# Kernel optimization log

Hardware: AMD Instinct MI355X
Metric: run time of the kernel (lower is better)

## Reference

```python
import jax, jax.numpy as jnp
import numpy as np

HID = 2048
NH = 16
HD = HID // NH  # 128
EPS = 1e-6
BASE = 10000.0


def _rmsnorm(x, w):
    xf = x.astype(jnp.float32)
    y = xf * jax.lax.rsqrt(jnp.mean(xf * xf, axis=-1, keepdims=True) + EPS)
    return y.astype(x.dtype) * w


def _rope_cos_sin(seq_len, dtype):
    inv_freq = 1.0 / (BASE ** (jnp.arange(0, HD, 2, dtype=jnp.float32) / HD))
    t = jnp.arange(seq_len, dtype=jnp.float32)
    freqs = jnp.outer(t, inv_freq)          # [S, HD/2]
    emb = jnp.concatenate([freqs, freqs], axis=-1)  # [S, HD]
    return jnp.cos(emb).astype(dtype), jnp.sin(emb).astype(dtype)


def _rotate_half(x):
    x1, x2 = jnp.split(x, 2, axis=-1)
    return jnp.concatenate([-x2, x1], axis=-1)


def setup_inputs() -> dict:
    key = jax.random.key(0)
    ks = jax.random.split(key, 8)
    B, S = 2, 2048
    s = 0.02
    return {
        "hidden_states": jax.random.normal(ks[0], (B, S, HID), jnp.float32),
        "Wq": jax.random.normal(ks[1], (HID, HID), jnp.float32) * s,
        "Wk": jax.random.normal(ks[2], (HID, HID), jnp.float32) * s,
        "Wv": jax.random.normal(ks[3], (HID, HID), jnp.float32) * s,
        "Wo": jax.random.normal(ks[4], (HID, HID), jnp.float32) * s,
        "w1": jax.random.normal(ks[5], (HID, HID), jnp.float32) * s,
        "w2": jax.random.normal(ks[6], (HID, HID), jnp.float32) * s,
        "w3": jax.random.normal(ks[7], (HID, HID), jnp.float32) * s,
        "ln1_w": jnp.ones((HID,), jnp.float32),
        "ln2_w": jnp.ones((HID,), jnp.float32),
    }


def reference(hidden_states, Wq, Wk, Wv, Wo, w1, w2, w3, ln1_w, ln2_w):
    B, S, _ = hidden_states.shape
    residual = hidden_states
    x = _rmsnorm(hidden_states, ln1_w)

    # projections -> [B, NH, S, HD]
    q = (x @ Wq).reshape(B, S, NH, HD).transpose(0, 2, 1, 3)
    k = (x @ Wk).reshape(B, S, NH, HD).transpose(0, 2, 1, 3)
    v = (x @ Wv).reshape(B, S, NH, HD).transpose(0, 2, 1, 3)

    cos, sin = _rope_cos_sin(S, x.dtype)  # [S, HD]
    cos = cos[None, None]  # broadcast over batch and heads
    sin = sin[None, None]
    q = q * cos + _rotate_half(q) * sin
    k = k * cos + _rotate_half(k) * sin

    scores = jnp.einsum("bhqd,bhkd->bhqk", q, k) / np.sqrt(HD).astype(np.float32)
    # no attention_mask (torch default path). fp32 softmax.
    attn = jax.nn.softmax(scores.astype(jnp.float32), axis=-1).astype(q.dtype)
    ctx = jnp.einsum("bhqk,bhkd->bhqd", attn, v)  # [B, NH, S, HD]
    ctx = ctx.transpose(0, 2, 1, 3).reshape(B, S, HID)
    attn_out = ctx @ Wo

    h = residual + attn_out
    residual = h
    y = _rmsnorm(h, ln2_w)
    mlp = (jax.nn.silu(y @ w1) * (y @ w3)) @ w2
    return residual + mlp
```

## Files before the change

### kernel.cpp

```cpp
#include <hip/hip_runtime.h>

#define HIDN 2048
#define NHEAD 16
#define HD 128
#define SEQ 2048
#define BATCH 2
#define NROWS (BATCH*SEQ)

typedef __bf16 bf16_t;
typedef bf16_t bf16x8 __attribute__((ext_vector_type(8)));
typedef float f32x4 __attribute__((ext_vector_type(4)));

#define AS1 __attribute__((address_space(1)))
#define AS3 __attribute__((address_space(3)))

__device__ __forceinline__ unsigned short f2bf(float x) {
  union { bf16_t b; unsigned short u; } cv; cv.b = (bf16_t)x; return cv.u;
}

#define MFMA16(a,b,c) __builtin_amdgcn_mfma_f32_16x16x32_bf16((a),(b),(c),0,0,0)

__device__ __forceinline__ void gload16(const void* g, void* l) {
  __builtin_amdgcn_global_load_lds((const AS1 void*)g, (AS3 void*)l, 16, 0, 0);
}

__global__ __launch_bounds__(256) void transpose_all_kernel(
    const float* __restrict__ Wq, const float* __restrict__ Wk,
    const float* __restrict__ Wv, const float* __restrict__ Wo,
    const float* __restrict__ w1, const float* __restrict__ w3,
    const float* __restrict__ w2, unsigned short* __restrict__ wblk) {
  const int z = blockIdx.z;
  const float* W; unsigned short* dstb; int tmode = 0, half = 0;
  switch (z) {
    case 0: W = Wq; dstb = wblk;                       tmode = 1; break;
    case 1: W = Wk; dstb = wblk + (size_t)2048 * HIDN; tmode = 1; break;
    case 2: W = Wv; dstb = wblk + (size_t)4096 * HIDN; break;
    case 3: W = Wo; dstb = wblk + (size_t)6144 * HIDN; break;
    case 4: W = w1; dstb = wblk + (size_t)8192 * HIDN; tmode = 2; half = 0; break;
    case 5: W = w3; dstb = wblk + (size_t)8192 * HIDN; tmode = 2; half = 1; break;
    default: W = w2; dstb = wblk + (size_t)12288 * HIDN; break;
  }
  __shared__ float t[64][69];
  const int tid = threadIdx.x;
  const int bn = blockIdx.x * 64, bk = blockIdx.y * 64;
  const int lc = (tid & 15) * 4, lrw = tid >> 4;
#pragma unroll
  for (int i = 0; i < 4; ++i) {
    int k = bk + lrw + i * 16;
    float4 v = *(const float4*)(W + (long)k * HIDN + bn + lc);
    t[lrw + i * 16][lc] = v.x; t[lrw + i * 16][lc + 1] = v.y;
    t[lrw + i * 16][lc + 2] = v.z; t[lrw + i * 16][lc + 3] = v.w;
  }
  __syncthreads();
  const int nl = tid >> 2, k0 = (tid & 3) * 16;
  int n = bn + nl;
  int dst;
  if (tmode == 0) dst = n;
  else if (tmode == 1) { int d = n & 127; dst = (n & ~127) | ((d & 63) << 1) | (d >> 6); }
  else dst = (n >> 4) * 32 + half * 16 + (n & 15);
  unsigned short* orow = dstb + (long)dst * HIDN + bk + k0;
#pragma unroll
  for (int j = 0; j < 16; j += 4) {
    ushort4 o;
    o.x = f2bf(t[k0 + j][nl]);     o.y = f2bf(t[k0 + j + 1][nl]);
    o.z = f2bf(t[k0 + j + 2][nl]); o.w = f2bf(t[k0 + j + 3][nl]);
    *(ushort4*)(orow + j) = o;
  }
}

__global__ void rope_table_kernel(float* __restrict__ cosT, float* __restrict__ sinT) {
  int s = blockIdx.x, d = threadIdx.x;
  float invf = powf(10000.0f, (-2.0f * (float)d) / 128.0f);
  float ang = (float)s * invf;
  cosT[s * 64 + d] = cosf(ang);
  sinT[s * 64 + d] = sinf(ang);
}

__global__ __launch_bounds__(256) void rmsnorm_kernel(
    const float* __restrict__ x, const float* __restrict__ w, unsigned short* __restrict__ out) {
  long row = blockIdx.x;
  const float* xr = x + row * HIDN;
  int c0 = threadIdx.x * 4;
  float4 v0 = *(const float4*)(xr + c0);
  float4 v1 = *(const float4*)(xr + 1024 + c0);
  float s = v0.x*v0.x + v0.y*v0.y + v0.z*v0.z + v0.w*v0.w
          + v1.x*v1.x + v1.y*v1.y + v1.z*v1.z + v1.w*v1.w;
#pragma unroll
  for (int off = 1; off < 64; off <<= 1) s += __shfl_xor(s, off);
  __shared__ float red[4];
  if ((threadIdx.x & 63) == 0) red[threadIdx.x >> 6] = s;
  __syncthreads();
  float tot = red[0] + red[1] + red[2] + red[3];
  float r = 1.0f / sqrtf(tot * (1.0f / (float)HIDN) + 1e-6f);
  float4 w0 = *(const float4*)(w + c0);
  float4 w1 = *(const float4*)(w + 1024 + c0);
  ushort4 o0, o1;
  o0.x = f2bf(v0.x * r * w0.x); o0.y = f2bf(v0.y * r * w0.y);
  o0.z = f2bf(v0.z * r * w0.z); o0.w = f2bf(v0.w * r * w0.w);
  o1.x = f2bf(v1.x * r * w1.x); o1.y = f2bf(v1.y * r * w1.y);
  o1.z = f2bf(v1.z * r * w1.z); o1.w = f2bf(v1.w * r * w1.w);
  *(ushort4*)(out + row * HIDN + c0) = o0;
  *(ushort4*)(out + row * HIDN + 1024 + c0) = o1;
}

template <int MODE>
__global__ __launch_bounds__(512, 2) void gemm256_kernel(
    const unsigned short* __restrict__ A, const unsigned short* __restrict__ Bt,
    int nbx,
    void* __restrict__ p0, void* __restrict__ p1, void* __restrict__ p2,
    const float* __restrict__ cosT, const float* __restrict__ sinT) {
  __shared__ unsigned short L[65536];
  const int tid = threadIdx.x;
  const int wave = tid >> 6, lane = tid & 63;
  const int lr = lane & 15, lkg = lane >> 4;
  const int wr = wave >> 2, wc = wave & 3;
  const int x7 = lr & 7;
  const int nwg = (int)gridDim.x;
  const int bid = (int)blockIdx.x;
  const int wg = (bid & 7) * (nwg >> 3) + (bid >> 3);
  const int bx = wg % nbx, by = wg / nbx;
  const long bm = (long)by * 256, bn = (long)bx * 256;
  const int sslot = (lane & 7) ^ (lane >> 3);
  const unsigned short* Ag = A + (bm + wave * 8 + (lane >> 3)) * HIDN + sslot * 8;
  const unsigned short* Bg = Bt + (bn + wave * 8 + (lane >> 3)) * HIDN + sslot * 8;
  const char* Lc = (const char*)L;
  f32x4 acc[8][4] = {};
  bf16x8 af[2][2], bfr[4][2];

#define STG(b, mat, half, tile)                                                   \
  {                                                                               \
    const unsigned short* gsrc = ((mat) ? Bg : Ag) + ((long)(half) * 128) * HIDN + (long)(tile) * 64; \
    unsigned short* ldst = &L[((4 * (b) + 2 * (mat) + (half)) * 8192) + wave * 8 * 64]; \
    gload16(gsrc, ldst);                                                          \
    gload16(gsrc + (long)64 * HIDN, ldst + 4096);                                 \
  }
#define DSRA(b, q)                                                                \
  { _Pragma("unroll") for (int mm = 0; mm < 2; ++mm) {                            \
      int row128 = ((q) * 2 + mm) * 16 + lr;                                      \
      _Pragma("unroll") for (int ks = 0; ks < 2; ++ks) {                          \
        int s = ks * 4 + lkg;                                                     \
        af[mm][ks] = *(const bf16x8*)(Lc + (4 * (b) + wr) * 16384 + row128 * 128 + ((s ^ x7) << 4)); \
      } } }
#define DSRB(b)                                                                   \
  { _Pragma("unroll") for (int n = 0; n < 4; ++n) {                               \
      int row128 = (wc & 1) * 64 + n * 16 + lr;                                   \
      _Pragma("unroll") for (int ks = 0; ks < 2; ++ks) {                          \
        int s = ks * 4 + lkg;                                                     \
        bfr[n][ks] = *(const bf16x8*)(Lc + (4 * (b) + 2 + (wc >> 1)) * 16384 + row128 * 128 + ((s ^ x7) << 4)); \
      } } }
#define MFMAQ(q)                                                                  \
  { __builtin_amdgcn_s_setprio(1);                                                \
    _Pragma("unroll") for (int mm = 0; mm < 2; ++mm)                              \
      _Pragma("unroll") for (int n = 0; n < 4; ++n) {                             \
        acc[(q) * 2 + mm][n] = MFMA16(af[mm][0], bfr[n][0], acc[(q) * 2 + mm][n]); \
        acc[(q) * 2 + mm][n] = MFMA16(af[mm][1], bfr[n][1], acc[(q) * 2 + mm][n]); \
      }                                                                           \
    __builtin_amdgcn_s_setprio(0); }
#define BARR __builtin_amdgcn_s_barrier()
#define LGK0 { asm volatile("s_waitcnt lgkmcnt(0)" ::: "memory"); __builtin_amdgcn_sched_barrier(0); }

  STG(0, 0, 0, 0); STG(0, 0, 1, 0); STG(0, 1, 0, 0); STG(0, 1, 1, 0);
  STG(1, 1, 0, 1); STG(1, 1, 1, 1); STG(1, 0, 0, 1);
  asm volatile("s_waitcnt vmcnt(6)" ::: "memory");
  __builtin_amdgcn_sched_barrier(0);
  BARR;

  const int NIT = HIDN / 128;
#pragma unroll 1
  for (int i = 0; i < NIT; ++i) {
    const int t2 = 2 * i + 2, t3 = 2 * i + 3;
    const bool nl_ = (i < NIT - 1);
    DSRA(0, 0); DSRB(0);
    STG(1, 0, 1, 2 * i + 1);
    asm volatile("s_waitcnt lgkmcnt(8)" ::: "memory");
    BARR; LGK0; MFMAQ(0); BARR;
    DSRA(0, 1);
    if (nl_) STG(0, 1, 0, t2);
    BARR; LGK0; MFMAQ(1); BARR;
    DSRA(0, 2);
    if (nl_) STG(0, 1, 1, t2);
    BARR; LGK0; MFMAQ(2); BARR;
    DSRA(0, 3);
    BARR; LGK0; MFMAQ(3);
    if (nl_) { asm volatile("s_waitcnt vmcnt(4)" ::: "memory"); }
    else     { asm volatile("s_waitcnt vmcnt(0)" ::: "memory"); }
    __builtin_amdgcn_sched_barrier(0);
    BARR;
    DSRA(1, 0); DSRB(1);
    if (nl_) STG(0, 0, 0, t2);
    asm volatile("s_waitcnt lgkmcnt(8)" ::: "memory");
    BARR; LGK0; MFMAQ(0); BARR;
    DSRA(1, 1);
    if (nl_) { STG(0, 0, 1, t2); STG(1, 1, 0, t3); }
    BARR; LGK0; MFMAQ(1); BARR;
    DSRA(1, 2);
    if (nl_) STG(1, 1, 1, t3);
    BARR; LGK0; MFMAQ(2); BARR;
    DSRA(1, 3);
    if (nl_) STG(1, 0, 0, t3);
    BARR; LGK0; MFMAQ(3);
    if (nl_) { asm volatile("s_waitcnt vmcnt(6)" ::: "memory"); __builtin_amdgcn_sched_barrier(0); }
    BARR;
  }
#undef STG
#undef DSRA
#undef DSRB
#undef MFMAQ
#undef BARR
#undef LGK0

  const int gc0 = (int)bn + wc * 64;
  if (MODE == 1) {
    unsigned short* bout = (unsigned short*)p0;
#pragma unroll
    for (int m = 0; m < 8; ++m) {
      long r0 = bm + wr * 128 + m * 16 + lkg * 4;
#pragma unroll
      for (int n = 0; n < 4; n += 2) {
        int ggrp = (gc0 + n * 16) >> 5;
        long c = (long)ggrp * 16 + lr;
#pragma unroll
        for (int r = 0; r < 4; ++r) {
          float x = acc[m][n][r], g = acc[m][n + 1][r];
          float sv = x / (1.0f + __expf(-x)) * g;
          bout[(r0 + r) * 2048 + c] = f2bf(sv);
        }
      }
    }
  } else {
    int bufid = gc0 >> 11;
    if (bufid == 2) {
      unsigned short* vT = (unsigned short*)p2;
#pragma unroll
      for (int m = 0; m < 8; ++m) {
        long r0 = bm + wr * 128 + m * 16 + lkg * 4;
        long bq = r0 >> 11;
        int s = (int)(r0 & 2047);
#pragma unroll
        for (int n = 0; n < 4; ++n) {
          int wcol = (gc0 + n * 16 + lr) & 2047;
          int hh = wcol >> 7, dd = wcol & 127;
          ushort4 pw;
          pw.x = f2bf(acc[m][n][0]); pw.y = f2bf(acc[m][n][1]);
          pw.z = f2bf(acc[m][n][2]); pw.w = f2bf(acc[m][n][3]);
          *(ushort4*)(vT + ((bq * 16 + hh) * 128 + dd) * (long)SEQ + s) = pw;
        }
      }
    } else {
      unsigned short* dst = (bufid == 0) ? (unsigned short*)p0 : (unsigned short*)p1;
      const float qscale = (bufid == 0) ? 0.08838834764831845f : 1.0f;
#pragma unroll
      for (int m = 0; m < 8; ++m) {
        long r0 = bm + wr * 128 + m * 16 + lkg * 4;
#pragma unroll
        for (int n = 0; n < 4; ++n) {
          int wcol = (gc0 + n * 16 + lr) & 2047;
          int f = wcol & 127, hh = wcol >> 7;
          int j = f >> 1, odd = f & 1;
          int oc = hh * 128 + (odd ? 64 : 0) + j;
#pragma unroll
          for (int r = 0; r < 4; ++r) {
            long row = r0 + r;
            int s = (int)(row & (SEQ - 1));
            float cv = cosT[s * 64 + j], sn = sinT[s * 64 + j];
            float v = acc[m][n][r];
            float o = __shfl_xor(v, 1);
            float res = (odd ? (v * cv + o * sn) : (v * cv - o * sn)) * qscale;
            dst[row * 2048 + oc] = f2bf(res);
          }
        }
      }
    }
  }
}

template <int MODE>
__global__ __launch_bounds__(256) void gemm_kernel(
    const unsigned short* __restrict__ A, const unsigned short* __restrict__ Bt, int N,
    void* __restrict__ p0, const void* __restrict__ p1) {
  __shared__ unsigned short As[128 * 32];
  __shared__ unsigned short Bs[128 * 32];
  const int tid = threadIdx.x;
  const int lane = tid & 63, wave = tid >> 6;
  const int wm = (wave >> 1) * 64, wn = (wave & 1) * 64;
  const int lr = lane & 15, lkg = lane >> 4;
  const long bm = (long)blockIdx.y * 128, bn = (long)blockIdx.x * 128;
  f32x4 acc[4][4] = {};
  const int rA0 = wave * 32 + (lane >> 2);
  const int gs0 = (lane & 3) ^ ((rA0 >> 1) & 3);
  const int gs1 = (lane & 3) ^ (((rA0 + 16) >> 1) & 3);
  const unsigned short* Ag0 = A + (bm + rA0) * HIDN + gs0 * 8;
  const unsigned short* Ag1 = A + (bm + rA0 + 16) * HIDN + gs1 * 8;
  const unsigned short* Bg0 = Bt + (bn + rA0) * HIDN + gs0 * 8;
  const unsigned short* Bg1 = Bt + (bn + rA0 + 16) * HIDN + gs1 * 8;
  unsigned short* lA0 = &As[(wave * 32) * 32];
  unsigned short* lA1 = &As[(wave * 32 + 16) * 32];
  unsigned short* lB0 = &Bs[(wave * 32) * 32];
  unsigned short* lB1 = &Bs[(wave * 32 + 16) * 32];
  for (int k0 = 0; k0 < HIDN; k0 += 32) {
    __syncthreads();
    gload16(Ag0 + k0, lA0);
    gload16(Ag1 + k0, lA1);
    gload16(Bg0 + k0, lB0);
    gload16(Bg1 + k0, lB1);
    __syncthreads();
    bf16x8 af[4], bfr[4];
#pragma unroll
    for (int m = 0; m < 4; ++m) {
      int row = wm + m * 16 + lr;
      af[m] = *(const bf16x8*)((const char*)As + row * 64 + ((lkg ^ ((row >> 1) & 3)) << 4));
    }
#pragma unroll
    for (int n = 0; n < 4; ++n) {
      int row = wn + n * 16 + lr;
      bfr[n] = *(const bf16x8*)((const char*)Bs + row * 64 + ((lkg ^ ((row >> 1) & 3)) << 4));
    }
#pragma unroll
    for (int m = 0; m < 4; ++m)
#pragma unroll
      for (int n = 0; n < 4; ++n) acc[m][n] = MFMA16(af[m], bfr[n], acc[m][n]);
  }
  float* fout = (float*)p0;
  const float* addsrc = (const float*)p1;
#pragma unroll
  for (int m = 0; m < 4; ++m)
#pragma unroll
    for (int n = 0; n < 4; ++n) {
      long r0 = bm + wm + m * 16 + lkg * 4;
      long c = bn + wn + n * 16 + lr;
#pragma unroll
      for (int r = 0; r < 4; ++r) {
        long idx = (r0 + r) * 2048 + c;
        if (MODE == 2) fout[idx] = addsrc[idx] + acc[m][n][r];
        else fout[idx] = fout[idx] + acc[m][n][r];
      }
    }
}

__global__ __launch_bounds__(256) void flash_attn_kernel(
    const unsigned short* __restrict__ Q, const unsigned short* __restrict__ Kb,
    const unsigned short* __restrict__ vT, unsigned short* __restrict__ O) {
  __shared__ unsigned short Ks[2][64 * 128];
  __shared__ unsigned short Vs[2][128 * 64];
  __shared__ unsigned short Ps[4][16][72];
  const int qt = blockIdx.x, h = blockIdx.y, b = blockIdx.z;
  const int tid = threadIdx.x, wave = tid >> 6, lane = tid & 63;
  const int lr = lane & 15, lkg = lane >> 4, lk = lkg * 8;
  const long rowbase = (long)b * SEQ;
  const int qrow0 = qt * 64 + wave * 16;
  bf16x8 aq[4];
#pragma unroll
  for (int ks = 0; ks < 4; ++ks)
    aq[ks] = *(const bf16x8*)(Q + (rowbase + qrow0 + lr) * HIDN + h * HD + ks * 32 + lk);
  const unsigned short* vbase = vT + ((long)(b * 16 + h) * 128) * SEQ;
  const int krl = lane >> 4;
  const int vrl = lane >> 3, vch = lane & 7;
  f32x4 acc[8] = {};
  float m_ = -3.0e38f, l_ = 0.f;

#define STAGEKV(t_, kv0_)                                                          \
  {                                                                                \
    _Pragma("unroll")                                                              \
    for (int j = 0; j < 4; ++j) {                                                  \
      int rl = wave * 16 + j * 4 + krl;                                            \
      int slot = (lane & 15) ^ (rl & 15);                                          \
      gload16(Kb + (rowbase + (kv0_) + rl) * HIDN + h * HD + slot * 8,             \
              &Ks[(t_) & 1][(wave * 16 + j * 4) * 128]);                           \
    }                                                                              \
    _Pragma("unroll")                                                              \
    for (int j = 0; j < 4; ++j) {                                                  \
      int dd = wave * 32 + j * 8 + vrl;                                            \
      int slot = vch ^ (dd & 7);                                                   \
      gload16(vbase + (long)dd * SEQ + (kv0_) + slot * 8,                          \
              &Vs[(t_) & 1][(wave * 32 + j * 8) * 64]);                            \
    }                                                                              \
  }

  STAGEKV(0, 0);

  for (int t = 0; t < SEQ / 64; ++t) {
    asm volatile("s_waitcnt vmcnt(0)" ::: "memory");
    asm volatile("s_barrier" ::: "memory");
    if (t + 1 < SEQ / 64) STAGEKV(t + 1, (long)(t + 1) * 64);
    const char* ksb = (const char*)Ks[t & 1];
    f32x4 sa[4] = {};
#pragma unroll
    for (int n = 0; n < 4; ++n) {
      int row = n * 16 + lr;
#pragma unroll
      for (int ks = 0; ks < 4; ++ks) {
        bf16x8 bk = *(const bf16x8*)(ksb + row * 256 + (((ks * 4 + lkg) ^ (row & 15)) << 4));
        sa[n] = MFMA16(bk, aq[ks], sa[n]);
      }
    }
    float pmax = sa[0][0];
#pragma unroll
    for (int n = 0; n < 4; ++n)
#pragma unroll
      for (int r = 0; r < 4; ++r) pmax = fmaxf(pmax, sa[n][r]);
    pmax = fmaxf(pmax, __shfl_xor(pmax, 16));
    pmax = fmaxf(pmax, __shfl_xor(pmax, 32));
    if (__all(pmax - m_ <= 8.0f)) {
      float psum = 0.f;
#pragma unroll
      for (int n = 0; n < 4; ++n)
#pragma unroll
        for (int r = 0; r < 4; ++r) {
          float p = __expf(sa[n][r] - m_);
          sa[n][r] = p;
          psum += p;
        }
      psum += __shfl_xor(psum, 16);
      psum += __shfl_xor(psum, 32);
      l_ += psum;
    } else {
      float mnew = fmaxf(m_, pmax);
      float corr = __expf(m_ - mnew);
      float psum = 0.f;
#pragma unroll
      for (int n = 0; n < 4; ++n)
#pragma unroll
        for (int r = 0; r < 4; ++r) {
          float p = __expf(sa[n][r] - mnew);
          sa[n][r] = p;
          psum += p;
        }
      psum += __shfl_xor(psum, 16);
      psum += __shfl_xor(psum, 32);
      l_ = l_ * corr + psum;
      m_ = mnew;
      float corr4[4];
#pragma unroll
      for (int r = 0; r < 4; ++r) corr4[r] = __shfl(corr, 4 * lkg + r);
#pragma unroll
      for (int df = 0; df < 8; ++df)
#pragma unroll
        for (int r = 0; r < 4; ++r) acc[df][r] *= corr4[r];
    }
#pragma unroll
    for (int n = 0; n < 4; ++n) {
      ushort4 pw;
      pw.x = f2bf(sa[n][0]); pw.y = f2bf(sa[n][1]);
      pw.z = f2bf(sa[n][2]); pw.w = f2bf(sa[n][3]);
      *(ushort4*)&Ps[wave][lr][n * 16 + 4 * lkg] = pw;
    }
    bf16x8 pa0 = *(const bf16x8*)&Ps[wave][lr][lk];
    bf16x8 pa1 = *(const bf16x8*)&Ps[wave][lr][32 + lk];
    const char* vsb = (const char*)Vs[t & 1];
#pragma unroll
    for (int df = 0; df < 8; ++df) {
      int row = df * 16 + lr;
      int x7 = row & 7;
      bf16x8 bv0 = *(const bf16x8*)(vsb + row * 128 + ((lkg ^ x7) << 4));
      bf16x8 bv1 = *(const bf16x8*)(vsb + row * 128 + (((4 + lkg) ^ x7) << 4));
      acc[df] = MFMA16(pa0, bv0, acc[df]);
      acc[df] = MFMA16(pa1, bv1, acc[df]);
    }
    asm volatile("s_barrier" ::: "memory");
  }
#undef STAGEKV
  float invl = 1.0f / l_;
  float invl4[4];
#pragma unroll
  for (int r = 0; r < 4; ++r) invl4[r] = __shfl(invl, 4 * lkg + r);
#pragma unroll
  for (int r = 0; r < 4; ++r) {
    long orow = rowbase + qrow0 + lkg * 4 + r;
#pragma unroll
    for (int df = 0; df < 8; ++df)
      O[orow * HIDN + h * HD + df * 16 + lr] = f2bf(acc[df][r] * invl4[r]);
  }
}

extern "C" void kernel_launch(void* const* d_in, const int* in_sizes, int n_in,
                              void* d_out, int out_size, void* d_ws, size_t ws_size,
                              hipStream_t stream) {
  const float* hidden = (const float*)d_in[0];
  const float* Wq = (const float*)d_in[1];
  const float* Wk = (const float*)d_in[2];
  const float* Wv = (const float*)d_in[3];
  const float* Wo = (const float*)d_in[4];
  const float* w1 = (const float*)d_in[5];
  const float* w2 = (const float*)d_in[6];
  const float* w3 = (const float*)d_in[7];
  const float* ln1 = (const float*)d_in[8];
  const float* ln2 = (const float*)d_in[9];
  float* out = (float*)d_out;

  char* ws = (char*)d_ws;
  size_t off = 0;
  auto alloc = [&](size_t bytes) -> void* {
    void* p = ws + off;
    off += (bytes + 255) & ~(size_t)255;
    return p;
  };
  unsigned short* wblk = (unsigned short*)alloc((size_t)(2048L * 6 + 2048) * HIDN * 2);
  unsigned short* wQ = wblk;
  unsigned short* wG = wblk + (size_t)8192 * HIDN;
  unsigned short* wO = wblk + (size_t)6144 * HIDN;
  unsigned short* wD = wblk + (size_t)12288 * HIDN;
  unsigned short* xb   = (unsigned short*)alloc((size_t)NROWS * HIDN * 2);
  unsigned short* qb   = (unsigned short*)alloc((size_t)NROWS * HIDN * 2);
  unsigned short* kb   = (unsigned short*)alloc((size_t)NROWS * HIDN * 2);
  unsigned short* vTb  = (unsigned short*)alloc((size_t)NROWS * HIDN * 2);
  unsigned short* ctxb = (unsigned short*)alloc((size_t)NROWS * HIDN * 2);
  float* cosT = (float*)alloc((size_t)SEQ * 64 * 4);
  float* sinT = (float*)alloc((size_t)SEQ * 64 * 4);
  if (off > ws_size) return;

  transpose_all_kernel<<<dim3(HIDN / 64, HIDN / 64, 7), 256, 0, stream>>>(
      Wq, Wk, Wv, Wo, w1, w3, w2, wblk);
  rope_table_kernel<<<SEQ, 64, 0, stream>>>(cosT, sinT);

  rmsnorm_kernel<<<NROWS, 256, 0, stream>>>(hidden, ln1, xb);

  gemm256_kernel<0><<<(6144 / 256) * (NROWS / 256), 512, 0, stream>>>(
      xb, wQ, 6144 / 256, qb, kb, vTb, cosT, sinT);

  flash_attn_kernel<<<dim3(SEQ / 64, NHEAD, BATCH), 256, 0, stream>>>(qb, kb, vTb, ctxb);

  gemm_kernel<2><<<dim3(2048 / 128, NROWS / 128), 256, 0, stream>>>(
      ctxb, wO, 2048, out, hidden);

  rmsnorm_kernel<<<NROWS, 256, 0, stream>>>(out, ln2, xb);

  gemm256_kernel<1><<<(4096 / 256) * (NROWS / 256), 512, 0, stream>>>(
      xb, wG, 4096 / 256, qb, nullptr, nullptr, nullptr, nullptr);

  gemm_kernel<3><<<dim3(2048 / 128, NROWS / 128), 256, 0, stream>>>(
      qb, wD, 2048, out, nullptr);
}
```

Baseline: 463.7 us.

## Restructure flash attention staging through registers, use exp2 softmax, remap blocks

Moves K/V staging off the direct global-to-LDS loads and onto register prefetch into a single LDS buffer. Shared memory is halved, and launch_bounds(256,3) asks for more resident blocks per CU. The Q scale now folds in log2(e), so softmax can use exp2f instead of __expf, and the rescale threshold is adjusted to match. Blocks are launched as a 1D grid with a remap that spreads consecutive block IDs across an 8-way interleave, likely for XCD/L2 locality. The trade-off is extra register pressure and an additional barrier per tile.

Result: no change. 463.6 us (-0.0%).

```diff
diff --git a/kernel.cpp b/kernel.cpp
--- a/kernel.cpp
+++ b/kernel.cpp
@@ -248,7 +248,7 @@
       }
     } else {
       unsigned short* dst = (bufid == 0) ? (unsigned short*)p0 : (unsigned short*)p1;
-      const float qscale = (bufid == 0) ? 0.08838834764831845f : 1.0f;
+      const float qscale = (bufid == 0) ? 0.12751689f : 1.0f;
 #pragma unroll
       for (int m = 0; m < 8; ++m) {
         long r0 = bm + wr * 128 + m * 16 + lkg * 4;
@@ -337,13 +337,15 @@
     }
 }
 
-__global__ __launch_bounds__(256) void flash_attn_kernel(
+__global__ __launch_bounds__(256, 3) void flash_attn_kernel(
     const unsigned short* __restrict__ Q, const unsigned short* __restrict__ Kb,
     const unsigned short* __restrict__ vT, unsigned short* __restrict__ O) {
-  __shared__ unsigned short Ks[2][64 * 128];
-  __shared__ unsigned short Vs[2][128 * 64];
+  __shared__ unsigned short Ks[64 * 128];
+  __shared__ unsigned short Vs[128 * 64];
   __shared__ unsigned short Ps[4][16][72];
-  const int qt = blockIdx.x, h = blockIdx.y, b = blockIdx.z;
+  const int bid = (int)blockIdx.x;
+  const int wg = (bid & 7) * 128 + (bid >> 3);
+  const int qt = wg & 31, h = (wg >> 5) & 15, b = wg >> 9;
   const int tid = threadIdx.x, wave = tid >> 6, lane = tid & 63;
   const int lr = lane & 15, lkg = lane >> 4, lk = lkg * 8;
   const long rowbase = (long)b * SEQ;
@@ -353,36 +355,41 @@
   for (int ks = 0; ks < 4; ++ks)
     aq[ks] = *(const bf16x8*)(Q + (rowbase + qrow0 + lr) * HIDN + h * HD + ks * 32 + lk);
   const unsigned short* vbase = vT + ((long)(b * 16 + h) * 128) * SEQ;
-  const int krl = lane >> 4;
-  const int vrl = lane >> 3, vch = lane & 7;
+  const int kr_ = tid >> 4, kc_ = tid & 15;
+  const int vd_ = tid >> 3, vc_ = tid & 7;
+  int4 kreg[4], vreg[4];
   f32x4 acc[8] = {};
   float m_ = -3.0e38f, l_ = 0.f;
 
-#define STAGEKV(t_, kv0_)                                                          \
-  {                                                                                \
+#define GLOADKV(kv0_)                                                              \
+  { _Pragma("unroll")                                                              \
+    for (int j = 0; j < 4; ++j)                                                    \
+      kreg[j] = *(const int4*)(Kb + (rowbase + (kv0_) + kr_ + j * 16) * HIDN + h * HD + kc_ * 8); \
     _Pragma("unroll")                                                              \
+    for (int j = 0; j < 4; ++j)                                                    \
+      vreg[j] = *(const int4*)(vbase + (long)(vd_ + j * 32) * SEQ + (kv0_) + vc_ * 8); }
+#define DSWRITEKV()                                                                \
+  { _Pragma("unroll")                                                              \
     for (int j = 0; j < 4; ++j) {                                                  \
-      int rl = wave * 16 + j * 4 + krl;                                            \
-      int slot = (lane & 15) ^ (rl & 15);                                          \
-      gload16(Kb + (rowbase + (kv0_) + rl) * HIDN + h * HD + slot * 8,             \
-              &Ks[(t_) & 1][(wave * 16 + j * 4) * 128]);                           \
+      int row = kr_ + j * 16;                                                      \
+      *(int4*)((char*)Ks + row * 256 + ((kc_ ^ (row & 15)) << 4)) = kreg[j];       \
     }                                                                              \
     _Pragma("unroll")                                                              \
     for (int j = 0; j < 4; ++j) {                                                  \
-      int dd = wave * 32 + j * 8 + vrl;                                            \
-      int slot = vch ^ (dd & 7);                                                   \
-      gload16(vbase + (long)dd * SEQ + (kv0_) + slot * 8,                          \
-              &Vs[(t_) & 1][(wave * 32 + j * 8) * 64]);                            \
-    }                                                                              \
-  }
-
-  STAGEKV(0, 0);
+      int d = vd_ + j * 32;                                                        \
+      *(int4*)((char*)Vs + d * 128 + ((vc_ ^ (d & 7)) << 4)) = vreg[j];            \
+    } }
+
+  GLOADKV(0);
+  asm volatile("s_waitcnt vmcnt(0)" ::: "memory");
+  DSWRITEKV();
+  asm volatile("s_waitcnt lgkmcnt(0)" ::: "memory");
+  __builtin_amdgcn_sched_barrier(0);
+  asm volatile("s_barrier" ::: "memory");
 
   for (int t = 0; t < SEQ / 64; ++t) {
-    asm volatile("s_waitcnt vmcnt(0)" ::: "memory");
-    asm volatile("s_barrier" ::: "memory");
-    if (t + 1 < SEQ / 64) STAGEKV(t + 1, (long)(t + 1) * 64);
-    const char* ksb = (const char*)Ks[t & 1];
+    if (t + 1 < SEQ / 64) GLOADKV((long)(t + 1) * 64);
+    const char* ksb = (const char*)Ks;
     f32x4 sa[4] = {};
 #pragma unroll
     for (int n = 0; n < 4; ++n) {
@@ -400,13 +407,13 @@
       for (int r = 0; r < 4; ++r) pmax = fmaxf(pmax, sa[n][r]);
     pmax = fmaxf(pmax, __shfl_xor(pmax, 16));
     pmax = fmaxf(pmax, __shfl_xor(pmax, 32));
-    if (__all(pmax - m_ <= 8.0f)) {
+    if (__all(pmax - m_ <= 11.54f)) {
       float psum = 0.f;
 #pragma unroll
       for (int n = 0; n < 4; ++n)
 #pragma unroll
         for (int r = 0; r < 4; ++r) {
-          float p = __expf(sa[n][r] - m_);
+          float p = exp2f(sa[n][r] - m_);
           sa[n][r] = p;
           psum += p;
         }
@@ -415,13 +422,13 @@
       l_ += psum;
     } else {
       float mnew = fmaxf(m_, pmax);
-      float corr = __expf(m_ - mnew);
+      float corr = exp2f(m_ - mnew);
       float psum = 0.f;
 #pragma unroll
       for (int n = 0; n < 4; ++n)
 #pragma unroll
         for (int r = 0; r < 4; ++r) {
-          float p = __expf(sa[n][r] - mnew);
+          float p = exp2f(sa[n][r] - mnew);
           sa[n][r] = p;
           psum += p;
         }
@@ -446,7 +453,7 @@
     }
     bf16x8 pa0 = *(const bf16x8*)&Ps[wave][lr][lk];
     bf16x8 pa1 = *(const bf16x8*)&Ps[wave][lr][32 + lk];
-    const char* vsb = (const char*)Vs[t & 1];
+    const char* vsb = (const char*)Vs;
 #pragma unroll
     for (int df = 0; df < 8; ++df) {
       int row = df * 16 + lr;
@@ -457,8 +464,16 @@
       acc[df] = MFMA16(pa1, bv1, acc[df]);
     }
     asm volatile("s_barrier" ::: "memory");
-  }
-#undef STAGEKV
+    if (t + 1 < SEQ / 64) {
+      asm volatile("s_waitcnt vmcnt(0)" ::: "memory");
+      DSWRITEKV();
+      asm volatile("s_waitcnt lgkmcnt(0)" ::: "memory");
+      __builtin_amdgcn_sched_barrier(0);
+      asm volatile("s_barrier" ::: "memory");
+    }
+  }
+#undef GLOADKV
+#undef DSWRITEKV
   float invl = 1.0f / l_;
   float invl4[4];
 #pragma unroll
@@ -517,7 +532,7 @@
   gemm256_kernel<0><<<(6144 / 256) * (NROWS / 256), 512, 0, stream>>>(
       xb, wQ, 6144 / 256, qb, kb, vTb, cosT, sinT);
 
-  flash_attn_kernel<<<dim3(SEQ / 64, NHEAD, BATCH), 256, 0, stream>>>(qb, kb, vTb, ctxb);
+  flash_attn_kernel<<<(SEQ / 64) * NHEAD * BATCH, 256, 0, stream>>>(qb, kb, vTb, ctxb);
 
   gemm_kernel<2><<<dim3(2048 / 128, NROWS / 128), 256, 0, stream>>>(
       ctxb, wO, 2048, out, hidden);
```
